# Kernel optimization log

Measured on AMD Instinct MI355X. Metric: run time of the kernel, lower is better.

Reference implementation:

```python
import jax, jax.numpy as jnp
import numpy as np

STRIDES = (8, 16, 32)
IMG = 640
REG_MAX = 16
TOPK = 10
ALPHA = 0.5
BETA = 6.0
EPS_IOU = 1e-16


def _make_anchors():
    # anchor centers for all pyramid levels, (N, 2) in pixel coords
    pts = []
    for s in STRIDES:
        h = w = IMG // s
        ys, xs = jnp.meshgrid(jnp.arange(h, dtype=jnp.float32),
                              jnp.arange(w, dtype=jnp.float32), indexing='ij')
        a = (jnp.stack([xs, ys], axis=-1).reshape(-1, 2) + 0.5) * s
        pts.append(a)
    return jnp.concatenate(pts, axis=0)  # (8400, 2)


def _iou_pairwise(pred, gt):
    # pred (B,N,4), gt (B,M,4) -> IoU (B,M,N)
    b1 = pred[:, None, :, :]   # (B,1,N,4)
    b2 = gt[:, :, None, :]     # (B,M,1,4)
    tl = jnp.maximum(b1[..., :2], b2[..., :2])
    br = jnp.minimum(b1[..., 2:], b2[..., 2:])
    wh = jnp.clip(br - tl, 0.0)
    inter = wh[..., 0] * wh[..., 1]
    a1 = (b1[..., 2] - b1[..., 0]) * (b1[..., 3] - b1[..., 1])
    a2 = (b2[..., 2] - b2[..., 0]) * (b2[..., 3] - b2[..., 1])
    return inter / (a1 + a2 - inter + EPS_IOU)


def _iou_1v1(b1, b2):
    # elementwise IoU, both (..., 4)
    tl = jnp.maximum(b1[..., :2], b2[..., :2])
    br = jnp.minimum(b1[..., 2:], b2[..., 2:])
    wh = jnp.clip(br - tl, 0.0)
    inter = wh[..., 0] * wh[..., 1]
    a1 = (b1[..., 2] - b1[..., 0]) * (b1[..., 3] - b1[..., 1])
    a2 = (b2[..., 2] - b2[..., 0]) * (b2[..., 3] - b2[..., 1])
    return inter / (a1 + a2 - inter + EPS_IOU)


def setup_inputs() -> dict:
    key = jax.random.key(0)
    ks = jax.random.split(key, 6)
    B, N, NC, M = 32, 8400, 80, 40
    pred_scores = jax.random.normal(ks[0], (B, N, NC), jnp.float32)
    pred_dist = jax.random.normal(ks[1], (B, N, 4 * REG_MAX), jnp.float32)
    gt_labels = jax.random.randint(ks[2], (B, M, 1), 0, NC, dtype=jnp.int32)
    cxy = jax.random.uniform(ks[3], (B, M, 2), jnp.float32) * 560.0 + 40.0
    wh = jax.random.uniform(ks[4], (B, M, 2), jnp.float32) * 120.0 + 20.0
    gt_bboxes = jnp.concatenate([jnp.clip(cxy - wh / 2, 0.0, float(IMG)),
                                 jnp.clip(cxy + wh / 2, 0.0, float(IMG))], axis=-1)
    dfl_weight = jax.random.normal(ks[5], (REG_MAX,), jnp.float32) * 0.05
    return {"pred_scores": pred_scores, "pred_dist": pred_dist,
            "gt_labels": gt_labels, "gt_bboxes": gt_bboxes,
            "dfl_weight": dfl_weight}


def reference(pred_scores, pred_dist, gt_labels, gt_bboxes, dfl_weight):
    B, N, NC = pred_scores.shape
    M = gt_bboxes.shape[1]
    anchors = _make_anchors()  # (N, 2)

    # DFL: softmax over reg bins, weighted sum with (random-init) conv weight
    prob = jax.nn.softmax(pred_dist.reshape(B, N, 4, REG_MAX), axis=-1)
    ltrb = prob @ dfl_weight                      # (B,N,4)
    pred_bboxes = jnp.concatenate([anchors - ltrb[..., :2],
                                   anchors + ltrb[..., 2:]], axis=-1)  # (B,N,4) xyxy

    # ---- task-aligned assigner (no-grad) ----
    sg = jax.lax.stop_gradient
    sig = jax.nn.sigmoid(sg(pred_scores))         # (B,N,NC)
    labels = gt_labels[..., 0].astype(jnp.int32)  # (B,M)
    sigT = jnp.swapaxes(sig, 1, 2)                # (B,NC,N)
    scores = jnp.take_along_axis(sigT, jnp.broadcast_to(labels[:, :, None], (B, M, N)), axis=1)  # (B,M,N)
    ious = jnp.clip(_iou_pairwise(sg(pred_bboxes), gt_bboxes), 0.0)      # (B,M,N)
    align = scores ** ALPHA * ious ** BETA        # (B,M,N)

    _, topk_idxs = jax.lax.top_k(align, TOPK)     # (B,M,TOPK) over anchors
    mask = jnp.zeros((B * M, N), dtype=align.dtype)
    mask = mask.at[jnp.arange(B * M)[:, None], topk_idxs.reshape(B * M, TOPK)].set(1.0)
    mask = mask.reshape(B, M, N)
    mask = mask * (align > 1e-9).astype(align.dtype)
    max_m = align.max(axis=1)                     # (B,N) best metric per anchor
    mask = mask * (align == max_m[:, None, :]).astype(align.dtype)

    fg_mask = mask.max(axis=1)                    # (B,N) in {0,1}
    tgt_idx = mask.argmax(axis=1)                 # (B,N) assigned gt index
    ts_sum = jnp.maximum(fg_mask.sum(), 1.0)

    # ---- classification targets (vectorized scatter) ----
    asg_labels = jnp.take_along_axis(labels, tgt_idx, axis=1)  # (B,N)
    target_scores = jax.nn.one_hot(asg_labels, NC, dtype=pred_scores.dtype) * (max_m * fg_mask)[..., None]

    x = pred_scores
    bce = jnp.maximum(x, 0.0) - x * target_scores + jnp.log1p(jnp.exp(-jnp.abs(x)))
    loss_cls = bce.sum() / ts_sum

    # ---- box IoU loss on positives (vectorized gather + mask) ----
    gt_asg = jnp.take_along_axis(gt_bboxes, tgt_idx[..., None], axis=1)  # (B,N,4)
    iou1 = _iou_1v1(pred_bboxes, gt_asg)          # (B,N)
    fg = fg_mask.sum()
    loss_box = jnp.where(fg > 0, ((1.0 - iou1) * fg_mask).sum() / fg, 0.0)

    return loss_cls + loss_box * 1.5
```

## Files before the change

kernel.cpp:

```cpp
#include <hip/hip_runtime.h>
#include <cstdint>
#include <cstddef>

#define BB 32
#define NN 8400
#define NCC 80
#define MM 40
#define RM 16
#define TOPKK 10
#define CAP 2048
#define SLOTP 41

__device__ __forceinline__ void anchor_xy(int n, float& ax, float& ay) {
    int s, x, y;
    if (n < 6400)      { s = 8;  y = n / 80;            x = n - y * 80; }
    else if (n < 8000) { int i = n - 6400; s = 16; y = i / 40; x = i - y * 40; }
    else               { int i = n - 8000; s = 32; y = i / 20; x = i - y * 20; }
    ax = ((float)x + 0.5f) * (float)s;
    ay = ((float)y + 0.5f) * (float)s;
}

__global__ __launch_bounds__(256) void k_main(const float* __restrict__ ps,
                                              const float* __restrict__ pd,
                                              const int*   __restrict__ gl,
                                              const float* __restrict__ gb,
                                              const float* __restrict__ w,
                                              float* __restrict__ pbb,
                                              float* __restrict__ maxm,
                                              int*   __restrict__ cnts,
                                              unsigned long long* __restrict__ lists,
                                              float* __restrict__ accum) {
    __shared__ float  sc[128 * SLOTP];
    __shared__ float4 box[128];
    __shared__ float  gtb[MM * 4];
    __shared__ int    glab[MM];
    __shared__ int    slotm[MM];
    __shared__ int    cmap[NCC];
    __shared__ float  cm[256];
    __shared__ float  redf[4];
    const int b  = blockIdx.y;
    const int n0 = blockIdx.x * 128;
    const int t  = threadIdx.x;

    if (t < MM * 4)              gtb[t] = gb[b * MM * 4 + t];
    if (t >= 192 && t < 192+MM)  glab[t - 192] = gl[b * MM + (t - 192)];
    if (t >= 64 && t < 64+NCC)   cmap[t - 64] = 0x7FFFFFFF;
    __syncthreads();
    if (t < MM) atomicMin(&cmap[glab[t]], t);
    __syncthreads();
    if (t < MM) slotm[t] = cmap[glab[t]];

    #pragma unroll
    for (int h = 0; h < 2; h++) {
        int f = t + h * 256;
        int a = f >> 2, side = f & 3;
        int nc = min(n0 + a, NN - 1);
        const float* p = pd + (((size_t)(b * NN + nc)) * 4 + side) * RM;
        float x[RM];
        #pragma unroll
        for (int i = 0; i < 4; i++) {
            float4 v = *(const float4*)(p + i * 4);
            x[i*4+0] = v.x; x[i*4+1] = v.y; x[i*4+2] = v.z; x[i*4+3] = v.w;
        }
        float mx = x[0];
        #pragma unroll
        for (int i = 1; i < RM; i++) mx = fmaxf(mx, x[i]);
        float s = 0.f, d = 0.f;
        #pragma unroll
        for (int i = 0; i < RM; i++) {
            float e = __builtin_amdgcn_exp2f((x[i] - mx) * 1.44269504f);
            s += e; d += e * w[i];
        }
        ((float*)box)[f] = d * __builtin_amdgcn_rcpf(s);
    }
    __syncthreads();
    if (t < 128) {
        int n = n0 + t;
        float ax, ay; anchor_xy(min(n, NN - 1), ax, ay);
        float4 v = box[t];
        float4 pb = make_float4(ax - v.x, ay - v.y, ax + v.z, ay + v.w);
        box[t] = pb;
        if (n < NN) *(float4*)(pbb + (size_t)(b * NN + n) * 4) = pb;
    }

    float4 vv[10];
    #pragma unroll
    for (int k = 0; k < 10; k++) {
        int f = t + k * 256;
        int row = f / 20, c4 = f - row * 20;
        int nc = min(n0 + row, NN - 1);
        vv[k] = *(const float4*)(ps + ((size_t)(b * NN + nc)) * NCC + c4 * 4);
    }
    float sp = 0.f;
    #pragma unroll
    for (int k = 0; k < 10; k++) {
        int f = t + k * 256;
        int row = f / 20, c4 = f - row * 20;
        float vmask = (n0 + row < NN) ? 1.f : 0.f;
        float xs[4] = {vv[k].x, vv[k].y, vv[k].z, vv[k].w};
        #pragma unroll
        for (int j = 0; j < 4; j++) {
            float x = xs[j];
            float e = __builtin_amdgcn_exp2f(-1.44269504f * fabsf(x));
            float r = __builtin_amdgcn_rcpf(1.0f + e);
            sp += vmask * (fmaxf(x, 0.f) + 0.69314718f * __builtin_amdgcn_logf(1.0f + e));
            int sl = cmap[c4 * 4 + j];
            if (sl < MM) sc[row * SLOTP + sl] = (x >= 0.f) ? r : e * r;
        }
    }
    __syncthreads();

    const int nloc = t & 127;
    const int n    = n0 + nloc;
    const int mb   = (t >> 7) * 20;
    const int lane = t & 63;
    const bool valid = (n < NN);
    float cmax = -INFINITY;
    float4 p4 = box[nloc];
    const float px1 = p4.x, py1 = p4.y, px2 = p4.z, py2 = p4.w;
    const float a1 = (px2 - px1) * (py2 - py1);
    #pragma unroll
    for (int j = 0; j < 20; j++) {
        int m = mb + j;
        float gx1 = gtb[m*4+0], gy1 = gtb[m*4+1], gx2 = gtb[m*4+2], gy2 = gtb[m*4+3];
        float a2 = (gx2 - gx1) * (gy2 - gy1);
        float iw = fmaxf(fminf(px2, gx2) - fmaxf(px1, gx1), 0.f);
        float ih = fmaxf(fminf(py2, gy2) - fmaxf(py1, gy1), 0.f);
        float inter = iw * ih;
        float iou = fmaxf(inter * __builtin_amdgcn_rcpf(a1 + a2 - inter + 1e-16f), 0.f);
        float al = 0.f;
        if (valid) {
            float sg = sc[nloc * SLOTP + slotm[m]];
            float i2 = iou * iou;
            al = __builtin_amdgcn_sqrtf(sg) * (i2 * i2 * i2);
        }
        cmax = fmaxf(cmax, al);
        bool pos = valid && (al > 1e-9f);
        unsigned long long msk = __ballot(pos);
        if (msk) {
            int leader = __ffsll((long long)msk) - 1;
            int basev = 0;
            if (lane == leader) basev = atomicAdd(&cnts[b * MM + m], __popcll(msk));
            basev = __shfl(basev, leader);
            if (pos) {
                int ofs = __popcll(msk & ((1ull << lane) - 1ull));
                int idx = basev + ofs;
                if (idx < CAP)
                    lists[((size_t)(b * MM + m)) * CAP + idx] =
                        ((unsigned long long)__float_as_uint(al) << 32) | (unsigned)n;
            }
        }
    }
    cm[t] = cmax;
    __syncthreads();
    if (t < 128 && valid) maxm[(size_t)b * NN + n] = fmaxf(cm[t], cm[t + 128]);

    #pragma unroll
    for (int off = 32; off > 0; off >>= 1) sp += __shfl_down(sp, off);
    if ((t & 63) == 0) redf[t >> 6] = sp;
    __syncthreads();
    if (t == 0) atomicAdd(accum, redf[0] + redf[1] + redf[2] + redf[3]);
}

__global__ __launch_bounds__(64) void k_topk(const unsigned long long* __restrict__ lists,
                                             const int*   __restrict__ cnts,
                                             const float* __restrict__ maxm,
                                             int* __restrict__ tgt) {
    __shared__ unsigned long long keys[CAP];
    __shared__ unsigned long long sel[TOPKK];
    const int bm = blockIdx.x, b = bm / MM, m = bm % MM, t = threadIdx.x;
    int cnt = min(cnts[bm], CAP);
    int kk = min(TOPKK, cnt);
    for (int i = t; i < cnt; i += 64) {
        unsigned long long L = lists[(size_t)bm * CAP + i];
        keys[i] = (L & 0xFFFFFFFF00000000ull) | (0xFFFFFFFFull - (L & 0xFFFFFFFFull));
    }
    __syncthreads();
    for (int p = 0; p < kk; p++) {
        unsigned long long best = 0ull;
        for (int i = t; i < cnt; i += 64) best = keys[i] > best ? keys[i] : best;
        #pragma unroll
        for (int off = 32; off > 0; off >>= 1) {
            unsigned long long o = __shfl_xor(best, off);
            best = o > best ? o : best;
        }
        for (int i = t; i < cnt; i += 64) if (keys[i] == best) keys[i] = 0ull;
        if (t == 0) sel[p] = best;
        __syncthreads();
    }
    if (t < kk) {
        unsigned long long bb = sel[t];
        float v = __uint_as_float((unsigned)(bb >> 32));
        int n = (int)(0xFFFFFFFFull - (bb & 0xFFFFFFFFull));
        if (v == maxm[(size_t)b * NN + n]) atomicMin(&tgt[(size_t)b * NN + n], m);
    }
}

__global__ __launch_bounds__(256) void k_fg(const int*   __restrict__ tgt,
                                            const int*   __restrict__ gl,
                                            const float* __restrict__ gb,
                                            const float* __restrict__ ps,
                                            const float* __restrict__ pbb,
                                            const float* __restrict__ maxm,
                                            float* __restrict__ accum) {
    int i = blockIdx.x * 256 + threadIdx.x;
    int t = threadIdx.x;
    float vdot = 0.f, vbox = 0.f, vfg = 0.f;
    int tg = tgt[i];
    if (tg < MM) {
        int b = i / NN;
        int lab = gl[b * MM + tg];
        float x = ps[(size_t)i * NCC + lab];
        float mm = maxm[i];
        float4 p = *(const float4*)(pbb + (size_t)i * 4);
        const float* g = gb + ((size_t)b * MM + tg) * 4;
        float a1 = (p.z - p.x) * (p.w - p.y);
        float a2 = (g[2] - g[0]) * (g[3] - g[1]);
        float iw = fmaxf(fminf(p.z, g[2]) - fmaxf(p.x, g[0]), 0.f);
        float ih = fmaxf(fminf(p.w, g[3]) - fmaxf(p.y, g[1]), 0.f);
        float inter = iw * ih;
        float iou = inter / (a1 + a2 - inter + 1e-16f);
        vdot = x * mm; vbox = 1.0f - iou; vfg = 1.0f;
    }
    #pragma unroll
    for (int off = 32; off > 0; off >>= 1) {
        vdot += __shfl_down(vdot, off);
        vbox += __shfl_down(vbox, off);
        vfg  += __shfl_down(vfg,  off);
    }
    __shared__ float r[3][4];
    if ((t & 63) == 0) { int wv = t >> 6; r[0][wv] = vdot; r[1][wv] = vbox; r[2][wv] = vfg; }
    __syncthreads();
    if (t < 3) {
        float s = r[t][0] + r[t][1] + r[t][2] + r[t][3];
        if (s != 0.f) atomicAdd(&accum[1 + t], s);
    }
}

__global__ void k_final(const float* __restrict__ accum, float* __restrict__ out) {
    float S0 = accum[0], dot = accum[1], box = accum[2], fg = accum[3];
    float ts = fmaxf(fg, 1.0f);
    float cls = (S0 - dot) / ts;
    float lb = (fg > 0.f) ? box / fg : 0.f;
    out[0] = cls + 1.5f * lb;
}

extern "C" void kernel_launch(void* const* d_in, const int* in_sizes, int n_in,
                              void* d_out, int out_size, void* d_ws, size_t ws_size,
                              hipStream_t stream) {
    const float* ps = (const float*)d_in[0];
    const float* pd = (const float*)d_in[1];
    const int*   gl = (const int*)  d_in[2];
    const float* gb = (const float*)d_in[3];
    const float* w  = (const float*)d_in[4];

    char* ws = (char*)d_ws;
    constexpr size_t PBB_BYTES  = (size_t)BB * NN * 4 * sizeof(float);
    constexpr size_t MAXM_BYTES = (size_t)BB * NN * sizeof(float);
    constexpr size_t TGT_BYTES  = (size_t)BB * NN * sizeof(int);
    constexpr size_t CNT_BYTES  = 8192;

    float* accum = (float*)ws;
    float* pbb   = (float*)(ws + 256);
    float* maxm  = (float*)(ws + 256 + PBB_BYTES);
    int*   tgt   = (int*)  (ws + 256 + PBB_BYTES + MAXM_BYTES);
    int*   cnts  = (int*)  (ws + 256 + PBB_BYTES + MAXM_BYTES + TGT_BYTES);
    unsigned long long* lists =
        (unsigned long long*)(ws + 256 + PBB_BYTES + MAXM_BYTES + TGT_BYTES + CNT_BYTES);

    hipMemsetAsync(accum, 0, 8 * sizeof(float), stream);
    hipMemsetAsync(tgt, 0x7F, TGT_BYTES, stream);
    hipMemsetAsync(cnts, 0, CNT_BYTES, stream);

    dim3 g3((NN + 127) / 128, BB);
    k_main<<<g3, 256, 0, stream>>>(ps, pd, gl, gb, w, pbb, maxm, cnts, lists, accum);
    k_topk<<<BB * MM, 64, 0, stream>>>(lists, cnts, maxm, tgt);
    k_fg<<<BB * NN / 256, 256, 0, stream>>>(tgt, gl, gb, ps, pbb, maxm, accum);
    k_final<<<1, 1, 0, stream>>>(accum, (float*)d_out);
}
```

Measured before the change: 197.7 us.

## Merge topk, fg and final kernels into one cooperative kernel with grid syncs

Replaces the top-k, foreground-gather and final kernels with a single cooperative launch of 1280 blocks of 256 threads. Two grid-wide syncs separate the phases. The top-k selection now uses 256 threads with a cross-wave reduction through shared memory. The large tgt memset is dropped because k_main now initialises tgt, and the accumulator and count memsets are merged into one. This removes several launches and memsets at the cost of grid-sync overhead and the need for all blocks to be co-resident.

After: 386.5 us. 1.95x slower.

```diff
diff --git a/kernel.cpp b/kernel.cpp
--- a/kernel.cpp
+++ b/kernel.cpp
@@ -1,4 +1,5 @@
 #include <hip/hip_runtime.h>
+#include <hip/hip_cooperative_groups.h>
 #include <cstdint>
 #include <cstddef>
 
@@ -29,7 +30,8 @@
                                               float* __restrict__ maxm,
                                               int*   __restrict__ cnts,
                                               unsigned long long* __restrict__ lists,
-                                              float* __restrict__ accum) {
+                                              float* __restrict__ accum,
+                                              int*   __restrict__ tgt) {
     __shared__ float  sc[128 * SLOTP];
     __shared__ float4 box[128];
     __shared__ float  gtb[MM * 4];
@@ -41,6 +43,8 @@
     const int b  = blockIdx.y;
     const int n0 = blockIdx.x * 128;
     const int t  = threadIdx.x;
+
+    if (t < 128 && n0 + t < NN) tgt[(size_t)b * NN + n0 + t] = 0x7F7F7F7F;
 
     if (t < MM * 4)              gtb[t] = gb[b * MM * 4 + t];
     if (t >= 192 && t < 192+MM)  glab[t - 192] = gl[b * MM + (t - 192)];
@@ -162,65 +166,76 @@
     if (t == 0) atomicAdd(accum, redf[0] + redf[1] + redf[2] + redf[3]);
 }
 
-__global__ __launch_bounds__(64) void k_topk(const unsigned long long* __restrict__ lists,
-                                             const int*   __restrict__ cnts,
-                                             const float* __restrict__ maxm,
-                                             int* __restrict__ tgt) {
+__global__ __launch_bounds__(256, 5) void k_post(const unsigned long long* __restrict__ lists,
+                                                 const int*   __restrict__ cnts,
+                                                 const float* __restrict__ maxm,
+                                                 int*         __restrict__ tgt,
+                                                 const int*   __restrict__ gl,
+                                                 const float* __restrict__ gb,
+                                                 const float* __restrict__ ps,
+                                                 const float* __restrict__ pbb,
+                                                 float*       __restrict__ accum,
+                                                 float*       __restrict__ out) {
     __shared__ unsigned long long keys[CAP];
     __shared__ unsigned long long sel[TOPKK];
-    const int bm = blockIdx.x, b = bm / MM, m = bm % MM, t = threadIdx.x;
+    __shared__ unsigned long long redu[4];
+    __shared__ float r[3][4];
+    const int t  = threadIdx.x;
+    const int bm = blockIdx.x;
+    const int b  = bm / MM, m = bm % MM;
+
     int cnt = min(cnts[bm], CAP);
     int kk = min(TOPKK, cnt);
-    for (int i = t; i < cnt; i += 64) {
+    for (int i = t; i < cnt; i += 256) {
         unsigned long long L = lists[(size_t)bm * CAP + i];
         keys[i] = (L & 0xFFFFFFFF00000000ull) | (0xFFFFFFFFull - (L & 0xFFFFFFFFull));
     }
     __syncthreads();
     for (int p = 0; p < kk; p++) {
         unsigned long long best = 0ull;
-        for (int i = t; i < cnt; i += 64) best = keys[i] > best ? keys[i] : best;
+        for (int i = t; i < cnt; i += 256) best = keys[i] > best ? keys[i] : best;
         #pragma unroll
         for (int off = 32; off > 0; off >>= 1) {
             unsigned long long o = __shfl_xor(best, off);
             best = o > best ? o : best;
         }
-        for (int i = t; i < cnt; i += 64) if (keys[i] == best) keys[i] = 0ull;
+        if ((t & 63) == 0) redu[t >> 6] = best;
+        __syncthreads();
+        best = redu[0];
+        #pragma unroll
+        for (int wv = 1; wv < 4; wv++) best = redu[wv] > best ? redu[wv] : best;
+        for (int i = t; i < cnt; i += 256) if (keys[i] == best) keys[i] = 0ull;
         if (t == 0) sel[p] = best;
         __syncthreads();
     }
     if (t < kk) {
-        unsigned long long bb = sel[t];
-        float v = __uint_as_float((unsigned)(bb >> 32));
-        int n = (int)(0xFFFFFFFFull - (bb & 0xFFFFFFFFull));
+        unsigned long long sv = sel[t];
+        float v = __uint_as_float((unsigned)(sv >> 32));
+        int n = (int)(0xFFFFFFFFull - (sv & 0xFFFFFFFFull));
         if (v == maxm[(size_t)b * NN + n]) atomicMin(&tgt[(size_t)b * NN + n], m);
     }
-}
-
-__global__ __launch_bounds__(256) void k_fg(const int*   __restrict__ tgt,
-                                            const int*   __restrict__ gl,
-                                            const float* __restrict__ gb,
-                                            const float* __restrict__ ps,
-                                            const float* __restrict__ pbb,
-                                            const float* __restrict__ maxm,
-                                            float* __restrict__ accum) {
-    int i = blockIdx.x * 256 + threadIdx.x;
-    int t = threadIdx.x;
+
+    cooperative_groups::this_grid().sync();
+
+    int i = bm * 256 + t;
     float vdot = 0.f, vbox = 0.f, vfg = 0.f;
-    int tg = tgt[i];
-    if (tg < MM) {
-        int b = i / NN;
-        int lab = gl[b * MM + tg];
-        float x = ps[(size_t)i * NCC + lab];
-        float mm = maxm[i];
-        float4 p = *(const float4*)(pbb + (size_t)i * 4);
-        const float* g = gb + ((size_t)b * MM + tg) * 4;
-        float a1 = (p.z - p.x) * (p.w - p.y);
-        float a2 = (g[2] - g[0]) * (g[3] - g[1]);
-        float iw = fmaxf(fminf(p.z, g[2]) - fmaxf(p.x, g[0]), 0.f);
-        float ih = fmaxf(fminf(p.w, g[3]) - fmaxf(p.y, g[1]), 0.f);
-        float inter = iw * ih;
-        float iou = inter / (a1 + a2 - inter + 1e-16f);
-        vdot = x * mm; vbox = 1.0f - iou; vfg = 1.0f;
+    if (i < BB * NN) {
+        int tg = tgt[i];
+        if (tg < MM) {
+            int bb2 = i / NN;
+            int lab = gl[bb2 * MM + tg];
+            float x = ps[(size_t)i * NCC + lab];
+            float mmv = maxm[i];
+            float4 p = *(const float4*)(pbb + (size_t)i * 4);
+            const float* g = gb + ((size_t)bb2 * MM + tg) * 4;
+            float a1 = (p.z - p.x) * (p.w - p.y);
+            float a2 = (g[2] - g[0]) * (g[3] - g[1]);
+            float iw = fmaxf(fminf(p.z, g[2]) - fmaxf(p.x, g[0]), 0.f);
+            float ih = fmaxf(fminf(p.w, g[3]) - fmaxf(p.y, g[1]), 0.f);
+            float inter = iw * ih;
+            float iou = inter / (a1 + a2 - inter + 1e-16f);
+            vdot = x * mmv; vbox = 1.0f - iou; vfg = 1.0f;
+        }
     }
     #pragma unroll
     for (int off = 32; off > 0; off >>= 1) {
@@ -228,21 +243,25 @@
         vbox += __shfl_down(vbox, off);
         vfg  += __shfl_down(vfg,  off);
     }
-    __shared__ float r[3][4];
     if ((t & 63) == 0) { int wv = t >> 6; r[0][wv] = vdot; r[1][wv] = vbox; r[2][wv] = vfg; }
     __syncthreads();
     if (t < 3) {
         float s = r[t][0] + r[t][1] + r[t][2] + r[t][3];
         if (s != 0.f) atomicAdd(&accum[1 + t], s);
     }
-}
-
-__global__ void k_final(const float* __restrict__ accum, float* __restrict__ out) {
-    float S0 = accum[0], dot = accum[1], box = accum[2], fg = accum[3];
-    float ts = fmaxf(fg, 1.0f);
-    float cls = (S0 - dot) / ts;
-    float lb = (fg > 0.f) ? box / fg : 0.f;
-    out[0] = cls + 1.5f * lb;
+
+    cooperative_groups::this_grid().sync();
+
+    if (bm == 0 && t == 0) {
+        float S0  = atomicAdd(&accum[0], 0.f);
+        float dot = atomicAdd(&accum[1], 0.f);
+        float box = atomicAdd(&accum[2], 0.f);
+        float fg  = atomicAdd(&accum[3], 0.f);
+        float ts = fmaxf(fg, 1.0f);
+        float cls = (S0 - dot) / ts;
+        float lb = (fg > 0.f) ? box / fg : 0.f;
+        out[0] = cls + 1.5f * lb;
+    }
 }
 
 extern "C" void kernel_launch(void* const* d_in, const int* in_sizes, int n_in,
@@ -255,26 +274,27 @@
     const float* w  = (const float*)d_in[4];
 
     char* ws = (char*)d_ws;
+    constexpr size_t ACC_BYTES  = 256;
+    constexpr size_t CNT_BYTES  = 8192;
     constexpr size_t PBB_BYTES  = (size_t)BB * NN * 4 * sizeof(float);
     constexpr size_t MAXM_BYTES = (size_t)BB * NN * sizeof(float);
     constexpr size_t TGT_BYTES  = (size_t)BB * NN * sizeof(int);
-    constexpr size_t CNT_BYTES  = 8192;
 
     float* accum = (float*)ws;
-    float* pbb   = (float*)(ws + 256);
-    float* maxm  = (float*)(ws + 256 + PBB_BYTES);
-    int*   tgt   = (int*)  (ws + 256 + PBB_BYTES + MAXM_BYTES);
-    int*   cnts  = (int*)  (ws + 256 + PBB_BYTES + MAXM_BYTES + TGT_BYTES);
+    int*   cnts  = (int*)  (ws + ACC_BYTES);
+    float* pbb   = (float*)(ws + ACC_BYTES + CNT_BYTES);
+    float* maxm  = (float*)(ws + ACC_BYTES + CNT_BYTES + PBB_BYTES);
+    int*   tgt   = (int*)  (ws + ACC_BYTES + CNT_BYTES + PBB_BYTES + MAXM_BYTES);
     unsigned long long* lists =
-        (unsigned long long*)(ws + 256 + PBB_BYTES + MAXM_BYTES + TGT_BYTES + CNT_BYTES);
-
-    hipMemsetAsync(accum, 0, 8 * sizeof(float), stream);
-    hipMemsetAsync(tgt, 0x7F, TGT_BYTES, stream);
-    hipMemsetAsync(cnts, 0, CNT_BYTES, stream);
+        (unsigned long long*)(ws + ACC_BYTES + CNT_BYTES + PBB_BYTES + MAXM_BYTES + TGT_BYTES);
+    float* outp = (float*)d_out;
+
+    hipMemsetAsync(ws, 0, ACC_BYTES + CNT_BYTES, stream);
 
     dim3 g3((NN + 127) / 128, BB);
-    k_main<<<g3, 256, 0, stream>>>(ps, pd, gl, gb, w, pbb, maxm, cnts, lists, accum);
-    k_topk<<<BB * MM, 64, 0, stream>>>(lists, cnts, maxm, tgt);
-    k_fg<<<BB * NN / 256, 256, 0, stream>>>(tgt, gl, gb, ps, pbb, maxm, accum);
-    k_final<<<1, 1, 0, stream>>>(accum, (float*)d_out);
+    k_main<<<g3, 256, 0, stream>>>(ps, pd, gl, gb, w, pbb, maxm, cnts, lists, accum, tgt);
+
+    void* args[] = { (void*)&lists, (void*)&cnts, (void*)&maxm, (void*)&tgt, (void*)&gl,
+                     (void*)&gb, (void*)&ps, (void*)&pbb, (void*)&accum, (void*)&outp };
+    hipLaunchCooperativeKernel((const void*)k_post, dim3(BB * MM), dim3(256), args, 0, stream);
 }
```
